# Kernel tuning notes

Hardware: AMD Instinct MI355X
Metric: run time of the kernel (lower is better)

The kernel has to match this reference:

```python
import jax, jax.numpy as jnp
import numpy as np

T, B, IN, M, BF = 256, 512, 128, 256, 2  # time(nodes), batch(trees), input, memory, branching


def setup_inputs() -> dict:
    key = jax.random.key(0)
    ks = jax.random.split(key, 13)
    s = 1.0 / np.sqrt(M)  # scale down the torch normal_ init to keep activations sane
    inputs = jax.random.normal(ks[0], (T, B, IN), jnp.float32)
    # valid tree encoding: repeat [leaf, leaf, binary-node]; stack pointer stays in-bounds
    pattern = np.tile(np.array([0, 0, 2], dtype=np.int32), T // 3 + 1)[:T]
    arities = jnp.broadcast_to(jnp.asarray(pattern)[:, None], (T, B)).astype(jnp.int32)
    d = dict(inputs=inputs, arities=arities)
    d["Wi"] = jax.random.normal(ks[1], (M, IN), jnp.float32) * s
    d["bi"] = jax.random.normal(ks[2], (M,), jnp.float32) * s
    d["Wo"] = jax.random.normal(ks[3], (M, IN), jnp.float32) * s
    d["bo"] = jax.random.normal(ks[4], (M,), jnp.float32) * s
    d["Wu"] = jax.random.normal(ks[5], (M, IN), jnp.float32) * s
    d["bu"] = jax.random.normal(ks[6], (M,), jnp.float32) * s
    d["Wf"] = jax.random.normal(ks[7], (M, IN), jnp.float32) * s
    d["bf_b"] = jax.random.normal(ks[8], (M,), jnp.float32) * s
    d["Ui"] = jax.random.normal(ks[9], (BF, M, M), jnp.float32) * s
    d["Uo"] = jax.random.normal(ks[10], (BF, M, M), jnp.float32) * s
    d["Uu"] = jax.random.normal(ks[11], (BF, M, M), jnp.float32) * s
    d["Uf"] = jax.random.normal(ks[12], (BF, M, M), jnp.float32) * s
    return d


def reference(inputs, arities, Wi, bi, Wo, bo, Wu, bu, Wf, bf_b, Ui, Uo, Uu, Uf):
    # NOTE: in the original torch code, fc_sum uses non-inplace .add() whose result is
    # discarded, so the forget-gate path (Wf/bf/Uf) never affects the output. We
    # faithfully reproduce that: c = sigmoid(i) * tanh(u).
    Tn, Bn = inputs.shape[0], inputs.shape[1]
    kB = jnp.arange(Bn)

    def unit(x, entries):
        gi = x @ Wi.T + bi
        go = x @ Wo.T + bo
        gu = x @ Wu.T + bu
        for k in range(BF):
            ch = entries[k][:, :M]  # child h part of [h, c]
            gi = gi + ch @ Ui[k].T
            go = go + ch @ Uo[k].T
            gu = gu + ch @ Uu[k].T
        c = jax.nn.sigmoid(gi) * jnp.tanh(gu)
        h = jax.nn.sigmoid(go) * jnp.tanh(c)
        return jnp.concatenate([h, c], axis=1)  # [B, 2M]

    memory0 = jnp.zeros((Tn, Bn, 2 * M), inputs.dtype)
    stack0 = jnp.zeros((Bn, Tn + BF), jnp.int32)
    sp0 = jnp.full((Bn,), BF - 1, jnp.int32)

    def step(carry, xs):
        memory, stack, sp = carry
        t, x, arity = xs
        entries = []
        for i in range(BF):
            idx = stack[kB, sp - i]          # [B] stack-based child gather
            e = memory[idx, kB]              # [B, 2M]
            mask = (arity > i).astype(memory.dtype)[:, None]
            entries.append(e * mask)
        ne = unit(x, entries)
        memory = memory.at[t].set(ne)
        sp = sp + 1 - jnp.abs(arity)
        ignore = arity == -1
        stack = stack.at[kB, sp].set(jnp.where(ignore, stack[kB, sp], t))
        return (memory, stack, sp), None

    ts = jnp.arange(Tn, dtype=jnp.int32)
    (memory, stack, sp), _ = jax.lax.scan(step, (memory0, stack0, sp0), (ts, inputs, arities))
    hc = memory[stack[kB, sp], kB]  # [B, 2M] root features
    return hc[:, :M], memory[:, :, :M]
```

## Files before the change

kernel.cpp:

```cpp
#include <hip/hip_runtime.h>
#include <cstdint>
#include <cstddef>


#define TT 256
#define BB 512
#define INN 128
#define MM 256
#define BFN 2
#define NLEVEL_LAUNCH 4
#define SL (TT + BFN)
#define KC 32

typedef __attribute__((ext_vector_type(8))) short bf16x8;
typedef __attribute__((ext_vector_type(8))) unsigned short ushort8;
typedef __attribute__((ext_vector_type(16))) float f32x16;

__device__ __forceinline__ unsigned short f2bf(float f) {
  unsigned u = __float_as_uint(f);
  unsigned r = u + 0x7fffu + ((u >> 16) & 1u);
  return (unsigned short)(r >> 16);
}

__device__ __forceinline__ float sigm_fast(float x) {
  return __builtin_amdgcn_rcpf(1.0f + __expf(-x));
}
__device__ __forceinline__ float tanh_fast(float x) {
  return 1.0f - 2.0f * __builtin_amdgcn_rcpf(1.0f + __expf(2.0f * x));
}

__device__ __forceinline__ void async16(unsigned short* lds,
                                        const unsigned short* g) {
  __builtin_amdgcn_global_load_lds(
      (const __attribute__((address_space(1))) unsigned int*)g,
      (__attribute__((address_space(3))) unsigned int*)lds, 16, 0, 0);
}

__global__ __launch_bounds__(32) void prep_sim(const int* __restrict__ ar,
                                               int* __restrict__ cidx,
                                               int* __restrict__ root) {
  __shared__ int st[32][SL];
  const int tid = threadIdx.x;
  const int b = blockIdx.x * 32 + tid;
  int* s = st[tid];
  for (int i = 0; i < SL; i++) s[i] = 0;
  int sp = BFN - 1;

  auto step = [&](int t, int a) {
    int2 cv;
    {
      int pos = sp;
      const int idx = s[pos];
      cv.x = (a > 0 && idx < t) ? idx : -1;
    }
    {
      int pos = sp - 1;
      if (pos < 0) pos += SL;
      const int idx = s[pos];
      cv.y = (a > 1 && idx < t) ? idx : -1;
    }
    *(int2*)&cidx[((size_t)t * BB + b) * BFN] = cv;
    const int aa = a < 0 ? -a : a;
    sp = sp + 1 - aa;
    if (sp < 0) sp += SL;
    if (sp >= SL) sp -= SL;
    if (a != -1) s[sp] = t;
  };

  int a0 = ar[b], a1 = ar[BB + b], a2 = ar[2 * BB + b], a3 = ar[3 * BB + b];
  for (int t = 0; t < TT; t += 4) {
    int n0 = 0, n1 = 0, n2 = 0, n3 = 0;
    if (t + 4 < TT) {
      n0 = ar[(size_t)(t + 4) * BB + b];
      n1 = ar[(size_t)(t + 5) * BB + b];
      n2 = ar[(size_t)(t + 6) * BB + b];
      n3 = ar[(size_t)(t + 7) * BB + b];
    }
    step(t, a0);
    step(t + 1, a1);
    step(t + 2, a2);
    step(t + 3, a3);
    a0 = n0; a1 = n1; a2 = n2; a3 = n3;
  }
  root[b] = s[sp];
}

__global__ __launch_bounds__(256) void prep_levels(const int* __restrict__ cidx,
                                                   int* __restrict__ order,
                                                   int* __restrict__ levelStart) {
  __shared__ int c0s[TT], c1s[TT], lv[TT];
  const int tid = threadIdx.x;
  if (tid < TT) {
    c0s[tid] = cidx[((size_t)tid * BB) * BFN + 0];
    c1s[tid] = cidx[((size_t)tid * BB) * BFN + 1];
    lv[tid] = 0;
  }
  __syncthreads();
  for (int it = 0; it < NLEVEL_LAUNCH - 1; it++) {
    int nl = 0;
    if (tid < TT) {
      const int c0 = c0s[tid], c1 = c1s[tid];
      if (c0 >= 0) nl = lv[c0] + 1;
      if (c1 >= 0) {
        const int v = lv[c1] + 1;
        if (v > nl) nl = v;
      }
    }
    __syncthreads();
    if (tid < TT) lv[tid] = nl;
    __syncthreads();
  }
  if (tid < TT) {
    const int l = lv[tid];
    int pos = 0;
    for (int j = 0; j < TT; j++) {
      const int lj = lv[j];
      pos += (lj < l || (lj == l && j < tid)) ? 1 : 0;
    }
    order[pos] = tid;
  }
  if (tid <= NLEVEL_LAUNCH) {
    int c = 0;
    for (int j = 0; j < TT; j++) c += (lv[j] < tid) ? 1 : 0;
    levelStart[tid] = c;
  }
}

__global__ __launch_bounds__(256) void conv_all(
    const float* __restrict__ x, const float* __restrict__ Wi,
    const float* __restrict__ Wo, const float* __restrict__ Wu,
    const float* __restrict__ Ui, const float* __restrict__ Uo,
    const float* __restrict__ Uu, unsigned short* __restrict__ wb,
    unsigned short* __restrict__ xb) {
  const int gid = blockIdx.x * 256 + threadIdx.x;
  const float* src;
  unsigned short* dst;
  size_t off;
  if (gid < 61440) {
    const int g8 = gid * 8;
    dst = wb + g8;
    if (g8 < 98304) {
      const int seg = g8 >> 15;
      off = g8 & 32767;
      src = (seg == 0) ? Wi : (seg == 1) ? Wo : Wu;
    } else {
      const int g2 = g8 - 98304;
      const int seg = g2 >> 17;
      off = g2 & 131071;
      src = (seg == 0) ? Ui : (seg == 1) ? Uo : Uu;
    }
  } else {
    off = ((size_t)(gid - 61440)) * 8;
    src = x;
    dst = xb + off;
  }
  const float4 v0 = *(const float4*)(src + off);
  const float4 v1 = *(const float4*)(src + off + 4);
  ushort8 o;
  o[0] = f2bf(v0.x); o[1] = f2bf(v0.y); o[2] = f2bf(v0.z); o[3] = f2bf(v0.w);
  o[4] = f2bf(v1.x); o[5] = f2bf(v1.y); o[6] = f2bf(v1.z); o[7] = f2bf(v1.w);
  *(ushort8*)dst = o;
}

__global__ __launch_bounds__(256, 3) void level_mfma(
    const unsigned short* __restrict__ xb, float* __restrict__ hf,
    unsigned short* __restrict__ hb, const float* __restrict__ bi,
    const float* __restrict__ bo, const float* __restrict__ bu,
    const unsigned short* __restrict__ wb, const int* __restrict__ cidx,
    const int* __restrict__ order, const int* __restrict__ levelStart,
    const int level) {
  const int s0 = levelStart[level];
  const int nt = levelStart[level + 1] - s0;
  if (nt <= 0) return;
  const int nTiles = nt * 16;
  const int xchunk = (nTiles + 7) >> 3;

  __shared__ __align__(16) unsigned short AW[2][10240];
  __shared__ int csh2[128][2];
  __shared__ int flagSh;

  const int tid = threadIdx.x;
  const int lane = tid & 63;
  const int w = tid >> 6;
  const int ln32 = lane & 31;
  const int lh = lane >> 5;
  const int bw = w & 1;
  const int mw = w >> 1;
  const int lrow = lane >> 2;
  const int skq = (lane & 3) ^ (lrow & 3);

  for (int it = blockIdx.x; it < (xchunk << 3); it += gridDim.x) {
    const int tile = (it & 7) * xchunk + (it >> 3);
    if (tile >= nTiles) continue;
    const int t = order[s0 + (tile >> 4)];
    const int sub = tile & 15;
    const int b0 = (sub >> 2) << 7;
    const int m0 = (sub & 3) << 6;

    __syncthreads();
    if (tid == 0) flagSh = 0;
    int fl = 0;
    if (tid < 128) {
      const int c0 = cidx[((size_t)t * BB + b0 + tid) * BFN + 0];
      const int c1 = cidx[((size_t)t * BB + b0 + tid) * BFN + 1];
      csh2[tid][0] = c0;
      csh2[tid][1] = c1;
      fl = (c0 >= 0 ? 1 : 0) | (c1 >= 0 ? 2 : 0);
    }
    {
#pragma unroll
      for (int u = 0; u < 2; u++) {
        const int j = w + u * 4;
        const int row = j * 16 + lrow;
        async16(&AW[0][j * 512],
                xb + (((size_t)t * BB + b0 + row) << 7) + skq * 8);
      }
#pragma unroll
      for (int u = 0; u < 3; u++) {
        const int jw = w + u * 4;
        const int roww = jw * 16 + lrow;
        const int g3 = roww >> 6;
        const int m = m0 + (roww & 63);
        async16(&AW[0][4096 + jw * 512],
                wb + g3 * 32768 + (size_t)m * INN + skq * 8);
      }
    }
    __syncthreads();
    if (fl) atomicOr(&flagSh, fl);
    const int rA0 = w * 16 + lrow;
    const int rA1 = (w + 4) * 16 + lrow;
    const int cA0 = csh2[rA0][0], cA1 = csh2[rA1][0];
    const int cB0 = csh2[rA0][1], cB1 = csh2[rA1][1];
    __syncthreads();
    const int pf = flagSh;
    const int nCh = 4 + ((pf & 1) ? 8 : 0) + ((pf & 2) ? 8 : 0);

    const int mcol = m0 + mw * 32 + ln32;
    const float vi = bi[mcol], vo = bo[mcol], vu = bu[mcol];
    f32x16 aI[2], aO[2], aU[2];
#pragma unroll
    for (int bt = 0; bt < 2; bt++)
#pragma unroll
      for (int r = 0; r < 16; r++) {
        aI[bt][r] = vi;
        aO[bt][r] = vo;
        aU[bt][r] = vu;
      }

    auto segk = [&](int ci, int& seg, int& k0) {
      if (ci < 4) {
        seg = 0;
        k0 = ci * KC;
      } else {
        const int j = ci - 4;
        if ((pf & 1) && j < 8) {
          seg = 1;
          k0 = j * KC;
        } else {
          seg = 2;
          k0 = ((pf & 1) ? j - 8 : j) * KC;
        }
      }
    };

    for (int i = 0; i < nCh; i++) {
      const int par = i & 1;
      if (i + 1 < nCh) {
        int seg, k0;
        segk(i + 1, seg, k0);
        unsigned short* buf = AW[1 - par];
        if (seg == 0) {
#pragma unroll
          for (int u = 0; u < 2; u++) {
            const int j = w + u * 4;
            const int row = j * 16 + lrow;
            async16(buf + j * 512,
                    xb + (((size_t)t * BB + b0 + row) << 7) + k0 + skq * 8);
          }
        } else {
#pragma unroll
          for (int u = 0; u < 2; u++) {
            const int j = w + u * 4;
            const int c = (seg == 1) ? (u ? cA1 : cA0) : (u ? cB1 : cB0);
            if (c >= 0) {
              const int row = j * 16 + lrow;
              async16(buf + j * 512,
                      hb + (((size_t)c * BB + b0 + row) << 8) + k0 + skq * 8);
            } else {
              const ushort8 z = {0, 0, 0, 0, 0, 0, 0, 0};
              *(ushort8*)(buf + j * 512 + lane * 8) = z;
            }
          }
        }
        {
          const unsigned short* wB;
          int Ks;
          if (seg == 0) {
            wB = wb;
            Ks = INN;
          } else {
            wB = wb + 98304 + (size_t)(seg - 1) * 65536;
            Ks = MM;
          }
#pragma unroll
          for (int u = 0; u < 3; u++) {
            const int jw = w + u * 4;
            const int roww = jw * 16 + lrow;
            const int g3 = roww >> 6;
            const int m = m0 + (roww & 63);
            const unsigned short* base =
                (Ks == INN) ? (wb + g3 * 32768) : (wB + (size_t)g3 * 131072);
            async16(buf + 4096 + jw * 512, base + (size_t)m * Ks + skq * 8 + k0);
          }
        }
      }

      {
        const unsigned short* buf = AW[par];
        const int r0 = bw * 64 + ln32;
        const int r1 = r0 + 32;
        const int rw = mw * 32 + ln32;
        const int sw3 = ln32 & 3;
#pragma unroll
        for (int ks = 0; ks < 2; ks++) {
          const int kq = ks * 2 + lh;
          const int sa = (kq ^ sw3) * 8;
          const bf16x8 a0 = *(const bf16x8*)(buf + r0 * 32 + sa);
          const bf16x8 a1 = *(const bf16x8*)(buf + r1 * 32 + sa);
          const bf16x8 bI = *(const bf16x8*)(buf + 4096 + rw * 32 + sa);
          const bf16x8 bO = *(const bf16x8*)(buf + 4096 + (64 + rw) * 32 + sa);
          const bf16x8 bU = *(const bf16x8*)(buf + 4096 + (128 + rw) * 32 + sa);
          aI[0] = __builtin_amdgcn_mfma_f32_32x32x16_bf16(a0, bI, aI[0], 0, 0, 0);
          aO[0] = __builtin_amdgcn_mfma_f32_32x32x16_bf16(a0, bO, aO[0], 0, 0, 0);
          aU[0] = __builtin_amdgcn_mfma_f32_32x32x16_bf16(a0, bU, aU[0], 0, 0, 0);
          aI[1] = __builtin_amdgcn_mfma_f32_32x32x16_bf16(a1, bI, aI[1], 0, 0, 0);
          aO[1] = __builtin_amdgcn_mfma_f32_32x32x16_bf16(a1, bO, aO[1], 0, 0, 0);
          aU[1] = __builtin_amdgcn_mfma_f32_32x32x16_bf16(a1, bU, aU[1], 0, 0, 0);
        }
      }
      if (i + 1 < nCh) __syncthreads();
    }

#pragma unroll
    for (int bt = 0; bt < 2; bt++) {
#pragma unroll
      for (int r = 0; r < 16; r++) {
        const int brow = b0 + bw * 64 + bt * 32 + (r & 3) + 8 * (r >> 2) + 4 * lh;
        const float gi = aI[bt][r];
        const float go = aO[bt][r];
        const float gu = aU[bt][r];
        const float c = sigm_fast(gi) * tanh_fast(gu);
        const float hv = sigm_fast(go) * tanh_fast(c);
        hf[((size_t)t * BB + brow) * MM + mcol] = hv;
        hb[(((size_t)t * BB + brow) << 8) + mcol] = f2bf(hv);
      }
    }
  }
}

__global__ __launch_bounds__(256) void root_gather(const float* __restrict__ h,
                                                   const int* __restrict__ root,
                                                   float* __restrict__ out) {
  const int idx = blockIdx.x * 256 + threadIdx.x;
  const int b = idx >> 8;
  const int m = idx & 255;
  out[idx] = h[((size_t)root[b] * BB + b) * MM + m];
}

extern "C" void kernel_launch(void* const* d_in, const int* in_sizes, int n_in,
                              void* d_out, int out_size, void* d_ws,
                              size_t ws_size, hipStream_t stream) {
  const float* x = (const float*)d_in[0];
  const int* ar = (const int*)d_in[1];
  const float* Wi = (const float*)d_in[2];
  const float* bi = (const float*)d_in[3];
  const float* Wo = (const float*)d_in[4];
  const float* bo = (const float*)d_in[5];
  const float* Wu = (const float*)d_in[6];
  const float* bu = (const float*)d_in[7];
  const float* Ui = (const float*)d_in[10];
  const float* Uo = (const float*)d_in[11];
  const float* Uu = (const float*)d_in[12];

  float* out = (float*)d_out;
  float* hf = out + (size_t)BB * MM;

  int* cidx = (int*)d_ws;
  int* root = cidx + (size_t)TT * BB * BFN;
  int* order = root + BB;
  int* levelStart = order + TT;
  unsigned short* wb = (unsigned short*)((char*)d_ws + 1051712);
  unsigned short* xb = (unsigned short*)((char*)d_ws + 2034752);
  unsigned short* hb = (unsigned short*)((char*)d_ws + 35589184);

  prep_sim<<<BB / 32, 32, 0, stream>>>(ar, cidx, root);
  prep_levels<<<1, 256, 0, stream>>>(cidx, order, levelStart);
  conv_all<<<8432, 256, 0, stream>>>(x, Wi, Wo, Wu, Ui, Uo, Uu, wb, xb);
  for (int lev = 0; lev < NLEVEL_LAUNCH; lev++) {
    level_mfma<<<4096, 256, 0, stream>>>(xb, hf, hb, bi, bo, bu, wb, cidx,
                                         order, levelStart, lev);
  }
  root_gather<<<(BB * MM) / 256, 256, 0, stream>>>(hf, root, out);
}
```

Baseline: 414.2 us.

## Triple-buffer LDS staging with one barrier per K-chunk and zero-buffer gathers

Moves the level GEMM's shared-memory staging from double to triple buffering. Each K-chunk now costs one barrier, gated by explicit vmcnt waits, and chunks are prefetched two steps ahead. The child-index shared table and its extra barriers are replaced by direct int2 loads plus a wave-level __any flag reduction. Missing children are now read asynchronously from a zero buffer in global memory, written by conv_all, instead of stored to LDS directly. The larger LDS footprint lowers the occupancy hint from 3 to 2 blocks per CU, and the hand-tuned waitcnt values carry correctness risk.

```diff
diff --git a/kernel.cpp b/kernel.cpp
--- a/kernel.cpp
+++ b/kernel.cpp
@@ -131,8 +131,15 @@
     const float* __restrict__ Wo, const float* __restrict__ Wu,
     const float* __restrict__ Ui, const float* __restrict__ Uo,
     const float* __restrict__ Uu, unsigned short* __restrict__ wb,
-    unsigned short* __restrict__ xb) {
+    unsigned short* __restrict__ xb, unsigned short* __restrict__ zb) {
   const int gid = blockIdx.x * 256 + threadIdx.x;
+  if (gid >= 2158592) {
+    if (gid < 2158592 + 64) {
+      const ushort8 z = {0, 0, 0, 0, 0, 0, 0, 0};
+      *(ushort8*)(zb + (size_t)(gid - 2158592) * 8) = z;
+    }
+    return;
+  }
   const float* src;
   unsigned short* dst;
   size_t off;
@@ -162,21 +169,20 @@
   *(ushort8*)dst = o;
 }
 
-__global__ __launch_bounds__(256, 3) void level_mfma(
+__global__ __launch_bounds__(256, 2) void level_mfma(
     const unsigned short* __restrict__ xb, float* __restrict__ hf,
     unsigned short* __restrict__ hb, const float* __restrict__ bi,
     const float* __restrict__ bo, const float* __restrict__ bu,
     const unsigned short* __restrict__ wb, const int* __restrict__ cidx,
     const int* __restrict__ order, const int* __restrict__ levelStart,
-    const int level) {
+    const unsigned short* __restrict__ zb, const int level) {
   const int s0 = levelStart[level];
   const int nt = levelStart[level + 1] - s0;
   if (nt <= 0) return;
   const int nTiles = nt * 16;
   const int xchunk = (nTiles + 7) >> 3;
 
-  __shared__ __align__(16) unsigned short AW[2][10240];
-  __shared__ int csh2[128][2];
+  __shared__ __align__(16) unsigned short AW[3 * 10240];
   __shared__ int flagSh;
 
   const int tid = threadIdx.x;
@@ -197,57 +203,22 @@
     const int b0 = (sub >> 2) << 7;
     const int m0 = (sub & 3) << 6;
 
+    if (tid == 0) flagSh = 0;
     __syncthreads();
-    if (tid == 0) flagSh = 0;
-    int fl = 0;
-    if (tid < 128) {
-      const int c0 = cidx[((size_t)t * BB + b0 + tid) * BFN + 0];
-      const int c1 = cidx[((size_t)t * BB + b0 + tid) * BFN + 1];
-      csh2[tid][0] = c0;
-      csh2[tid][1] = c1;
-      fl = (c0 >= 0 ? 1 : 0) | (c1 >= 0 ? 2 : 0);
-    }
-    {
-#pragma unroll
-      for (int u = 0; u < 2; u++) {
-        const int j = w + u * 4;
-        const int row = j * 16 + lrow;
-        async16(&AW[0][j * 512],
-                xb + (((size_t)t * BB + b0 + row) << 7) + skq * 8);
-      }
-#pragma unroll
-      for (int u = 0; u < 3; u++) {
-        const int jw = w + u * 4;
-        const int roww = jw * 16 + lrow;
-        const int g3 = roww >> 6;
-        const int m = m0 + (roww & 63);
-        async16(&AW[0][4096 + jw * 512],
-                wb + g3 * 32768 + (size_t)m * INN + skq * 8);
-      }
-    }
-    __syncthreads();
-    if (fl) atomicOr(&flagSh, fl);
+
     const int rA0 = w * 16 + lrow;
-    const int rA1 = (w + 4) * 16 + lrow;
-    const int cA0 = csh2[rA0][0], cA1 = csh2[rA1][0];
-    const int cB0 = csh2[rA0][1], cB1 = csh2[rA1][1];
-    __syncthreads();
-    const int pf = flagSh;
-    const int nCh = 4 + ((pf & 1) ? 8 : 0) + ((pf & 2) ? 8 : 0);
-
+    const int rA1 = rA0 + 64;
+    const int2 ca = *(const int2*)&cidx[((size_t)t * BB + b0 + rA0) * BFN];
+    const int2 cb = *(const int2*)&cidx[((size_t)t * BB + b0 + rA1) * BFN];
+    const int cA0 = ca.x, cB0 = ca.y, cA1 = cb.x, cB1 = cb.y;
     const int mcol = m0 + mw * 32 + ln32;
     const float vi = bi[mcol], vo = bo[mcol], vu = bu[mcol];
-    f32x16 aI[2], aO[2], aU[2];
-#pragma unroll
-    for (int bt = 0; bt < 2; bt++)
-#pragma unroll
-      for (int r = 0; r < 16; r++) {
-        aI[bt][r] = vi;
-        aO[bt][r] = vo;
-        aU[bt][r] = vu;
-      }
-
-    auto segk = [&](int ci, int& seg, int& k0) {
+    __builtin_amdgcn_sched_barrier(0);
+
+    int pf = 0;
+
+    auto stage_chunk = [&](int ci, unsigned short* buf) {
+      int seg, k0;
       if (ci < 4) {
         seg = 0;
         k0 = ci * KC;
@@ -261,62 +232,79 @@
           k0 = ((pf & 1) ? j - 8 : j) * KC;
         }
       }
+      if (seg == 0) {
+#pragma unroll
+        for (int u = 0; u < 2; u++) {
+          const int j = w + u * 4;
+          const int row = j * 16 + lrow;
+          async16(buf + j * 512,
+                  xb + (((size_t)t * BB + b0 + row) << 7) + k0 + skq * 8);
+        }
+      } else {
+#pragma unroll
+        for (int u = 0; u < 2; u++) {
+          const int j = w + u * 4;
+          const int c = (seg == 1) ? (u ? cA1 : cA0) : (u ? cB1 : cB0);
+          const int row = j * 16 + lrow;
+          const unsigned short* src =
+              (c >= 0)
+                  ? hb + (((size_t)c * BB + b0 + row) << 8) + k0 + skq * 8
+                  : zb + lane * 8;
+          async16(buf + j * 512, src);
+        }
+      }
+      {
+        const unsigned short* wB = wb + 98304 + (size_t)(seg - 1) * 65536;
+#pragma unroll
+        for (int u = 0; u < 3; u++) {
+          const int jw = w + u * 4;
+          const int roww = jw * 16 + lrow;
+          const int g3 = roww >> 6;
+          const int m = m0 + (roww & 63);
+          const unsigned short* base =
+              (seg == 0) ? (wb + g3 * 32768 + (size_t)m * INN)
+                         : (wB + (size_t)g3 * 131072 + (size_t)m * MM);
+          async16(buf + 4096 + jw * 512, base + k0 + skq * 8);
+        }
+      }
     };
 
+    stage_chunk(0, AW);
+    stage_chunk(1, AW + 10240);
+
+    int fl = 0;
+    if (__any(cA0 >= 0 || cA1 >= 0)) fl |= 1;
+    if (__any(cB0 >= 0 || cB1 >= 0)) fl |= 2;
+    if (lane == 0 && fl) atomicOr(&flagSh, fl);
+    asm volatile("s_waitcnt lgkmcnt(0)" ::: "memory");
+    __builtin_amdgcn_s_barrier();
+    __builtin_amdgcn_sched_barrier(0);
+    pf = flagSh;
+    const int nCh = 4 + ((pf & 1) ? 8 : 0) + ((pf & 2) ? 8 : 0);
+
+    f32x16 aI[2], aO[2], aU[2];
+#pragma unroll
+    for (int bt = 0; bt < 2; bt++)
+#pragma unroll
+      for (int r = 0; r < 16; r++) {
+        aI[bt][r] = vi;
+        aO[bt][r] = vo;
+        aU[bt][r] = vu;
+      }
+
+    int cur = 0, nxt2 = 2;
     for (int i = 0; i < nCh; i++) {
-      const int par = i & 1;
-      if (i + 1 < nCh) {
-        int seg, k0;
-        segk(i + 1, seg, k0);
-        unsigned short* buf = AW[1 - par];
-        if (seg == 0) {
-#pragma unroll
-          for (int u = 0; u < 2; u++) {
-            const int j = w + u * 4;
-            const int row = j * 16 + lrow;
-            async16(buf + j * 512,
-                    xb + (((size_t)t * BB + b0 + row) << 7) + k0 + skq * 8);
-          }
-        } else {
-#pragma unroll
-          for (int u = 0; u < 2; u++) {
-            const int j = w + u * 4;
-            const int c = (seg == 1) ? (u ? cA1 : cA0) : (u ? cB1 : cB0);
-            if (c >= 0) {
-              const int row = j * 16 + lrow;
-              async16(buf + j * 512,
-                      hb + (((size_t)c * BB + b0 + row) << 8) + k0 + skq * 8);
-            } else {
-              const ushort8 z = {0, 0, 0, 0, 0, 0, 0, 0};
-              *(ushort8*)(buf + j * 512 + lane * 8) = z;
-            }
-          }
-        }
-        {
-          const unsigned short* wB;
-          int Ks;
-          if (seg == 0) {
-            wB = wb;
-            Ks = INN;
-          } else {
-            wB = wb + 98304 + (size_t)(seg - 1) * 65536;
-            Ks = MM;
-          }
-#pragma unroll
-          for (int u = 0; u < 3; u++) {
-            const int jw = w + u * 4;
-            const int roww = jw * 16 + lrow;
-            const int g3 = roww >> 6;
-            const int m = m0 + (roww & 63);
-            const unsigned short* base =
-                (Ks == INN) ? (wb + g3 * 32768) : (wB + (size_t)g3 * 131072);
-            async16(buf + 4096 + jw * 512, base + (size_t)m * Ks + skq * 8 + k0);
-          }
-        }
-      }
+      if (i + 1 < nCh)
+        asm volatile("s_waitcnt vmcnt(5) lgkmcnt(0)" ::: "memory");
+      else
+        asm volatile("s_waitcnt vmcnt(0) lgkmcnt(0)" ::: "memory");
+      __builtin_amdgcn_s_barrier();
+      __builtin_amdgcn_sched_barrier(0);
+
+      if (i + 2 < nCh) stage_chunk(i + 2, AW + nxt2 * 10240);
 
       {
-        const unsigned short* buf = AW[par];
+        const unsigned short* buf = AW + cur * 10240;
         const int r0 = bw * 64 + ln32;
         const int r1 = r0 + 32;
         const int rw = mw * 32 + ln32;
@@ -338,7 +326,8 @@
           aU[1] = __builtin_amdgcn_mfma_f32_32x32x16_bf16(a1, bU, aU[1], 0, 0, 0);
         }
       }
-      if (i + 1 < nCh) __syncthreads();
+      cur = (cur == 2) ? 0 : cur + 1;
+      nxt2 = (nxt2 == 2) ? 0 : nxt2 + 1;
     }
 
 #pragma unroll
@@ -392,13 +381,14 @@
   unsigned short* wb = (unsigned short*)((char*)d_ws + 1051712);
   unsigned short* xb = (unsigned short*)((char*)d_ws + 2034752);
   unsigned short* hb = (unsigned short*)((char*)d_ws + 35589184);
+  unsigned short* zb = (unsigned short*)((char*)d_ws + 102698048);
 
   prep_sim<<<BB / 32, 32, 0, stream>>>(ar, cidx, root);
   prep_levels<<<1, 256, 0, stream>>>(cidx, order, levelStart);
-  conv_all<<<8432, 256, 0, stream>>>(x, Wi, Wo, Wu, Ui, Uo, Uu, wb, xb);
+  conv_all<<<8433, 256, 0, stream>>>(x, Wi, Wo, Wu, Ui, Uo, Uu, wb, xb, zb);
   for (int lev = 0; lev < NLEVEL_LAUNCH; lev++) {
     level_mfma<<<4096, 256, 0, stream>>>(xb, hf, hb, bi, bo, bu, wb, cidx,
-                                         order, levelStart, lev);
+                                         order, levelStart, zb, lev);
   }
   root_gather<<<(BB * MM) / 256, 256, 0, stream>>>(hf, root, out);
 }
```

Result: faster. 403.2 us (-2.6%).
